# Performance work log

Measured on AMD Instinct MI355X. Metric: run time of the kernel, lower is better.

## Reference

```python
import jax, jax.numpy as jnp
import numpy as np

V, E, M, Q, K_ANS, L = 100000, 300, 256, 64, 1024, 64
T = K_ANS * L
WINDOW_SIZES = (1, 2, 3, 4, 5)


def setup_inputs() -> dict:
    key = jax.random.key(0)
    ks = jax.random.split(key, 16)
    s = 0.05
    inp = {
        "data_q": jax.random.randint(ks[0], (Q,), 0, V, dtype=jnp.int32),
        "data_as_word": jax.random.randint(ks[1], (T,), 0, V, dtype=jnp.int32),
        "sizes": jnp.full((K_ANS,), L, dtype=jnp.int32),
        "emb": jax.random.normal(ks[2], (V, E), jnp.float32) * s,
        "W1": jax.random.normal(ks[3], (E, M), jnp.float32) * s,
        "b1": jnp.zeros((M,), jnp.float32),
        "W2": jax.random.normal(ks[4], (E, M), jnp.float32) * s,
        "b2": jnp.zeros((M,), jnp.float32),
        "Wl": jax.random.normal(ks[5], (len(WINDOW_SIZES) * M, M), jnp.float32) * s,
        "bl": jnp.zeros((M,), jnp.float32),
        "Ws": jax.random.normal(ks[6], (M, 1), jnp.float32) * s,
        "bs": jnp.zeros((1,), jnp.float32),
    }
    for i, w in enumerate(WINDOW_SIZES):
        inp[f"Wc{i+1}"] = jax.random.normal(ks[7 + i], (M, M, w), jnp.float32) * s
        inp[f"bc{i+1}"] = jnp.zeros((M,), jnp.float32)
    return inp


def _dmax(c, sizes, w):
    # Dynamic max pool: c is [Lc, M] conv+relu over the concatenated answer axis;
    # each answer k owns conv positions [start_k, start_k + sizes_k - w + 1).
    starts = jnp.concatenate([jnp.zeros((1,), sizes.dtype), jnp.cumsum(sizes)[:-1]])
    pos = jnp.arange(c.shape[0])
    seg = jnp.searchsorted(starts, pos, side="right") - 1  # answer id per position
    valid = pos < starts[seg] + sizes[seg] - (w - 1)
    vals = jnp.where(valid[:, None], c, -jnp.inf)
    return jax.ops.segment_max(vals, seg, num_segments=sizes.shape[0])  # [K, M]


def reference(data_q, data_as_word, sizes, emb, W1, b1, W2, b2,
              Wc1, bc1, Wc2, bc2, Wc3, bc3, Wc4, bc4, Wc5, bc5, Wl, bl, Ws, bs):
    # Gated projection layer: sigmoid(Wx) * tanh(Wx)
    proj = lambda x: jax.nn.sigmoid(x @ W1 + b1) * jnp.tanh(x @ W2 + b2)
    q_p = proj(emb[data_q])        # [Q, M]
    a_p = proj(emb[data_as_word])  # [T, M]
    # Attention: mm -> softmax over dim 0 of attention.T -> mm (as in original)
    att = q_p @ a_p.T                       # [Q, T]
    w_att = jax.nn.softmax(att.T, axis=0)   # [T, Q]
    ctx = w_att @ q_p                       # [T, M]
    sim = a_p * ctx                         # compare step ('mul')  [T, M]
    # Conv + dynamic max pooling per window size
    x = sim.T[None]                         # [1, M, T]
    convs = ((Wc1, bc1), (Wc2, bc2), (Wc3, bc3), (Wc4, bc4), (Wc5, bc5))
    pools = []
    for wsz, (Wc, bc) in zip(WINDOW_SIZES, convs):
        c = jax.lax.conv_general_dilated(
            x, Wc, (1,), "VALID", dimension_numbers=("NCH", "OIH", "NCH"))[0].T  # [T-w+1, M]
        c = jax.nn.relu(c + bc)
        pools.append(_dmax(c, sizes, wsz))  # [K, M]
    h = jnp.tanh(jnp.concatenate(pools, axis=1) @ Wl + bl)  # [K, M]
    logits = (h @ Ws + bs).reshape(-1)                       # [K]
    return jax.nn.log_softmax(logits, axis=0)
```

## Files before the change

kernel.cpp:

```cpp
#include <hip/hip_runtime.h>

typedef unsigned short u16;
typedef unsigned int u32;
using s16x8 = __attribute__((ext_vector_type(8))) short;
using f32x4 = __attribute__((ext_vector_type(4))) float;
using u16x4 = __attribute__((ext_vector_type(4))) u16;

#define DEV __device__ __forceinline__

DEV u16 f2bf(float f) {
    u32 u = __builtin_bit_cast(u32, f);
    u32 r = (u + 0x7FFFu + ((u >> 16) & 1u)) >> 16;
    return (u16)r;
}
DEV float bf2f(u16 h) { return __builtin_bit_cast(float, ((u32)h) << 16); }

DEV f32x4 mfma16(s16x8 a, s16x8 b, f32x4 c) {
    return __builtin_amdgcn_mfma_f32_16x16x32_bf16(a, b, c, 0, 0, 0);
}

#define GLOAD(g, l) __builtin_amdgcn_global_load_lds( \
    (const __attribute__((address_space(1))) unsigned int*)(g), \
    (__attribute__((address_space(3))) unsigned int*)(l), 16, 0, 0)

__global__ void k_prep(const float* W1, const float* W2, const float* Wl,
                       const float* Wc1, const float* Wc2, const float* Wc3,
                       const float* Wc4, const float* Wc5,
                       u16* WpT, u16* WlT, u16* WcT) {
    int idx = blockIdx.x * 256 + threadIdx.x;
    if (idx < 512 * 320) {
        int n = idx / 320, k = idx - n * 320;
        float v = 0.f;
        if (k < 300) v = (n < 256) ? W1[k * 256 + n] : W2[k * 256 + (n - 256)];
        WpT[idx] = f2bf(v);
    } else if (idx < 512 * 320 + 256 * 1280) {
        int j2 = idx - 512 * 320;
        int m = j2 / 1280, j = j2 - m * 1280;
        WlT[j2] = f2bf(Wl[j * 256 + m]);
    } else {
        int j3 = idx - (512 * 320 + 256 * 1280);
        if (j3 < 983040) {
            int wsz; int off;
            if (j3 < 65536)       { wsz = 1; off = 0; }
            else if (j3 < 196608) { wsz = 2; off = 65536; }
            else if (j3 < 393216) { wsz = 3; off = 196608; }
            else if (j3 < 655360) { wsz = 4; off = 393216; }
            else                  { wsz = 5; off = 655360; }
            int loc = j3 - off;
            int o = loc / (256 * wsz);
            int kk = loc - o * (256 * wsz);
            int dw = kk >> 8, i = kk & 255;
            const float* W = (wsz == 1) ? Wc1 : (wsz == 2) ? Wc2 : (wsz == 3) ? Wc3
                             : (wsz == 4) ? Wc4 : Wc5;
            WcT[j3] = f2bf(W[(o * 256 + i) * wsz + dw]);
        }
    }
}

__global__ void k_starts(const int* sizes, int* starts) {
    __shared__ int s[1024];
    int t = threadIdx.x;
    int v = sizes[t];
    s[t] = v;
    __syncthreads();
    for (int off = 1; off < 1024; off <<= 1) {
        int add = (t >= off) ? s[t - off] : 0;
        __syncthreads();
        s[t] += add;
        __syncthreads();
    }
    starts[t] = s[t] - v;
}

__launch_bounds__(512)
__global__ void k_proj(const int* idx, const float* emb, const u16* WpT,
                       const float* b1, const float* b2, u16* out) {
    __shared__ u16 X[64 * 320];
    int tid = threadIdx.x;
    long row0 = (long)blockIdx.x * 64;
    {
        int r = tid >> 3, part = tid & 7;
        const float* src = emb + (long)idx[row0 + r] * 300;
        char* xrow = (char*)X + r * 640;
        u32 swz = (u32)((r & 7) << 4);
        for (int c0 = part * 40; c0 < part * 40 + 40; c0 += 4) {
            float4 f;
            if (c0 + 4 <= 300) f = *(const float4*)(src + c0);
            else {
                f.x = (c0 < 300) ? src[c0] : 0.f;
                f.y = (c0 + 1 < 300) ? src[c0 + 1] : 0.f;
                f.z = (c0 + 2 < 300) ? src[c0 + 2] : 0.f;
                f.w = (c0 + 3 < 300) ? src[c0 + 3] : 0.f;
            }
            u16x4 h = { f2bf(f.x), f2bf(f.y), f2bf(f.z), f2bf(f.w) };
            *(u16x4*)(xrow + ((u32)(c0 * 2) ^ swz)) = h;
        }
    }
    __syncthreads();
    int wv = tid >> 6, lane = tid & 63, l15 = lane & 15, lq = lane >> 4;
    f32x4 acc[4][4] = {};
    for (int s = 0; s < 10; ++s) {
        s16x8 a[4], b[4];
#pragma unroll
        for (int c = 0; c < 4; ++c) {
            int mt = 2 * wv + (c & 1) + (c >> 1) * 16;
            int o = mt * 16 + l15;
            a[c] = *(const s16x8*)(WpT + o * 320 + s * 32 + lq * 8);
        }
#pragma unroll
        for (int nt = 0; nt < 4; ++nt) {
            int r = nt * 16 + l15;
            b[nt] = *(const s16x8*)((const char*)X + r * 640 +
                                    ((u32)(s * 64 + lq * 16) ^ ((u32)(r & 7) << 4)));
        }
#pragma unroll
        for (int c = 0; c < 4; ++c)
#pragma unroll
            for (int nt = 0; nt < 4; ++nt)
                acc[c][nt] = mfma16(a[c], b[nt], acc[c][nt]);
    }
    __syncthreads();
    u16* Y = X;
#pragma unroll
    for (int c = 0; c < 2; ++c) {
        int o0 = (2 * wv + c) * 16 + lq * 4;
#pragma unroll
        for (int nt = 0; nt < 4; ++nt) {
            int t = nt * 16 + l15;
#pragma unroll
            for (int r = 0; r < 4; ++r) {
                float xs = acc[c][nt][r] + b1[o0 + r];
                float xt = acc[c + 2][nt][r] + b2[o0 + r];
                float v = (1.f / (1.f + __expf(-xs))) * tanhf(xt);
                Y[t * 256 + o0 + r] = f2bf(v);
            }
        }
    }
    __syncthreads();
    for (int j = tid; j < 2048; j += 512) {
        int t = j >> 5, c8 = (j & 31) * 8;
        *(s16x8*)(out + (row0 + t) * 256 + c8) = *(const s16x8*)(Y + t * 256 + c8);
    }
}

__launch_bounds__(256)
__global__ void k_att(const u16* qp, const u16* ap, float* att) {
    __shared__ u16 Q[64 * 256];
    __shared__ u16 A[64 * 256];
    int tid = threadIdx.x;
    long t0 = (long)blockIdx.x * 64;
    for (int j = tid; j < 2048; j += 256) {
        int r = j >> 5, c8 = (j & 31) * 8;
        u32 dst = (u32)(c8 * 2) ^ ((u32)(r & 7) << 4);
        *(s16x8*)((char*)Q + r * 512 + dst) = *(const s16x8*)(qp + r * 256 + c8);
        *(s16x8*)((char*)A + r * 512 + dst) = *(const s16x8*)(ap + (t0 + r) * 256 + c8);
    }
    __syncthreads();
    int wv = tid >> 6, lane = tid & 63, l15 = lane & 15, lq = lane >> 4;
    f32x4 acc[4] = {};
    for (int s = 0; s < 8; ++s) {
        int brow = wv * 16 + l15;
        s16x8 b = *(const s16x8*)((const char*)A + brow * 512 +
                                  ((u32)(s * 64 + lq * 16) ^ ((u32)(brow & 7) << 4)));
#pragma unroll
        for (int mt = 0; mt < 4; ++mt) {
            int arow = mt * 16 + l15;
            s16x8 a = *(const s16x8*)((const char*)Q + arow * 512 +
                                      ((u32)(s * 64 + lq * 16) ^ ((u32)(arow & 7) << 4)));
            acc[mt] = mfma16(a, b, acc[mt]);
        }
    }
#pragma unroll
    for (int mt = 0; mt < 4; ++mt) {
        long t = t0 + wv * 16 + l15;
        *(f32x4*)(att + t * 64 + mt * 16 + lq * 4) = acc[mt];
    }
}

__global__ void k_red1(const float* att, float* partm, float* parts) {
    int tid = threadIdx.x;
    int q = tid & 63, sub = tid >> 6;
    long t0 = (long)blockIdx.x * 512;
    float m = -3.0e38f, s = 0.f;
    for (int i = sub; i < 512; i += 4) {
        float v = att[(t0 + i) * 64 + q];
        if (v > m) { s = s * __expf(m - v) + 1.f; m = v; }
        else s += __expf(v - m);
    }
    __shared__ float Lm[4][64], Ls[4][64];
    Lm[sub][q] = m; Ls[sub][q] = s;
    __syncthreads();
    if (sub == 0) {
        for (int i = 1; i < 4; ++i) {
            float m2 = Lm[i][q], s2 = Ls[i][q];
            float mn = fmaxf(m, m2);
            s = s * __expf(m - mn) + s2 * __expf(m2 - mn);
            m = mn;
        }
        partm[blockIdx.x * 64 + q] = m;
        parts[blockIdx.x * 64 + q] = s;
    }
}

__global__ void k_red2(const float* partm, const float* parts, float* mx, float* rden) {
    int q = threadIdx.x;
    float m = -3.0e38f, s = 0.f;
    for (int b = 0; b < 128; ++b) {
        float m2 = partm[b * 64 + q], s2 = parts[b * 64 + q];
        float mn = fmaxf(m, m2);
        s = s * __expf(m - mn) + s2 * __expf(m2 - mn);
        m = mn;
    }
    mx[q] = m;
    rden[q] = 1.f / s;
}

__launch_bounds__(256)
__global__ void k_ctx(const float* att, const float* mx, const float* rden,
                      const u16* qp, const u16* ap, u16* sim) {
    __shared__ u16 P[64 * 64];
    __shared__ u16 QT[256 * 64];
    __shared__ u16 Y[64 * 264];
    __shared__ float MX[64], RD[64];
    int tid = threadIdx.x;
    long t0 = (long)blockIdx.x * 64;
    if (tid < 64) { MX[tid] = mx[tid]; RD[tid] = rden[tid]; }
    {
        int m = tid;
        char* row = (char*)QT + m * 128;
        u32 swz = (u32)((m & 7) << 4);
        for (int q = 0; q < 64; ++q)
            *(u16*)(row + ((u32)(q * 2) ^ swz)) = qp[q * 256 + m];
    }
    __syncthreads();
    {
        int t = tid >> 2, qq = tid & 3;
        const float* arow = att + (t0 + t) * 64 + qq * 16;
        char* prow = (char*)P + t * 128;
        u32 swz = (u32)((t & 7) << 4);
#pragma unroll
        for (int i4 = 0; i4 < 4; ++i4) {
            float4 fv = *(const float4*)(arow + i4 * 4);
            int q0 = qq * 16 + i4 * 4;
            float p0 = __expf(fv.x - MX[q0 + 0]) * RD[q0 + 0];
            float p1 = __expf(fv.y - MX[q0 + 1]) * RD[q0 + 1];
            float p2 = __expf(fv.z - MX[q0 + 2]) * RD[q0 + 2];
            float p3 = __expf(fv.w - MX[q0 + 3]) * RD[q0 + 3];
            *(u16*)(prow + ((u32)((q0 + 0) * 2) ^ swz)) = f2bf(p0);
            *(u16*)(prow + ((u32)((q0 + 1) * 2) ^ swz)) = f2bf(p1);
            *(u16*)(prow + ((u32)((q0 + 2) * 2) ^ swz)) = f2bf(p2);
            *(u16*)(prow + ((u32)((q0 + 3) * 2) ^ swz)) = f2bf(p3);
        }
    }
    __syncthreads();
    int wv = tid >> 6, lane = tid & 63, l15 = lane & 15, lq = lane >> 4;
    f32x4 acc[16] = {};
#pragma unroll
    for (int s = 0; s < 2; ++s) {
        int arow = wv * 16 + l15;
        s16x8 a = *(const s16x8*)((const char*)P + arow * 128 +
                                  ((u32)(s * 64 + lq * 16) ^ ((u32)(arow & 7) << 4)));
#pragma unroll
        for (int nt = 0; nt < 16; ++nt) {
            int br = nt * 16 + l15;
            s16x8 b = *(const s16x8*)((const char*)QT + br * 128 +
                                      ((u32)(s * 64 + lq * 16) ^ ((u32)(br & 7) << 4)));
            acc[nt] = mfma16(a, b, acc[nt]);
        }
    }
#pragma unroll
    for (int nt = 0; nt < 16; ++nt) {
        int m = nt * 16 + l15;
        int t = wv * 16 + lq * 4;
#pragma unroll
        for (int r = 0; r < 4; ++r) Y[(t + r) * 264 + m] = f2bf(acc[nt][r]);
    }
    __syncthreads();
    for (int j = tid; j < 2048; j += 256) {
        int t = j >> 5, c8 = (j & 31) * 8;
        s16x8 y = *(const s16x8*)(Y + t * 264 + c8);
        s16x8 a8 = *(const s16x8*)(ap + (t0 + t) * 256 + c8);
        s16x8 o;
#pragma unroll
        for (int e = 0; e < 8; ++e)
            o[e] = (short)f2bf(bf2f((u16)a8[e]) * bf2f((u16)y[e]));
        *(s16x8*)(sim + (t0 + t) * 256 + c8) = o;
    }
}

__launch_bounds__(512)
__global__ void k_conv(const u16* sim, const u16* WcT,
                       const int* starts, const int* sizes,
                       const float* bc1, const float* bc2, const float* bc3,
                       const float* bc4, const float* bc5,
                       u16* pools, int Ttot) {
    __shared__ u16 LB[2][32768];
    int tid = threadIdx.x;
    int wv = tid >> 6, lane = tid & 63, l15 = lane & 15, lq = lane >> 4;
    int wm = wv >> 2, wn = wv & 3;
    int b = blockIdx.x;
    long s0 = starts[4 * b];
    int row8 = lane >> 3, seg = lane & 7;
    u32 sA = ((u32)(seg * 16)) ^ (((u32)(row8 & 7)) << 4);

    auto STAGE = [&](int nb, int w_, int dw_, int ic_) {
        int Krow = 256 * w_;
        long wbase = 65536L * ((w_ * (w_ - 1)) / 2);
#pragma unroll
        for (int it = 0; it < 4; ++it) {
            int c = wv * 4 + it;
            long g = s0 + dw_ + c * 8 + row8;
            if (g >= Ttot) g = Ttot - 1;
            const char* srcA = (const char*)sim + g * 512 + ic_ * 128 + sA;
            GLOAD(srcA, (char*)LB[nb] + c * 1024);
        }
#pragma unroll
        for (int it = 0; it < 4; ++it) {
            int c = wv * 4 + it;
            int o = c * 8 + row8;
            const char* srcB = (const char*)WcT +
                2L * (wbase + (long)o * Krow + dw_ * 256 + ic_ * 64) + sA;
            GLOAD(srcB, (char*)LB[nb] + 32768 + c * 1024);
        }
    };
    auto ADV = [](int& w_, int& dw_, int& ic_) {
        if (++ic_ == 4) { ic_ = 0; if (++dw_ == w_) { dw_ = 0; ++w_; } }
    };

    int wS = 1, dwS = 0, icS = 0;
    STAGE(0, wS, dwS, icS);
    ADV(wS, dwS, icS);
    __syncthreads();

    int buf = 0;
    f32x4 acc[8][4] = {};
    int wC = 1, dwC = 0, icC = 0;
    for (int t = 0; t < 60; ++t) {
        if (t < 59) { STAGE(buf ^ 1, wS, dwS, icS); ADV(wS, dwS, icS); }
        const char* Ab = (const char*)LB[buf];
        const char* Bb = (const char*)LB[buf] + 32768;
#pragma unroll
        for (int ks = 0; ks < 2; ++ks) {
            s16x8 A8[8], B4[4];
#pragma unroll
            for (int mt = 0; mt < 8; ++mt) {
                int row = wm * 128 + mt * 16 + l15;
                A8[mt] = *(const s16x8*)(Ab + row * 128 +
                          (((u32)(ks * 64 + lq * 16)) ^ (((u32)(row & 7)) << 4)));
            }
#pragma unroll
            for (int nt = 0; nt < 4; ++nt) {
                int o = wn * 64 + nt * 16 + l15;
                B4[nt] = *(const s16x8*)(Bb + o * 128 +
                          (((u32)(ks * 64 + lq * 16)) ^ (((u32)(o & 7)) << 4)));
            }
            __builtin_amdgcn_s_setprio(1);
#pragma unroll
            for (int mt = 0; mt < 8; ++mt)
#pragma unroll
                for (int nt = 0; nt < 4; ++nt)
                    acc[mt][nt] = mfma16(A8[mt], B4[nt], acc[mt][nt]);
            __builtin_amdgcn_s_setprio(0);
        }
        if (++icC == 4) {
            icC = 0;
            if (++dwC == wC) {
                dwC = 0;
                const float* bc = (wC == 1) ? bc1 : (wC == 2) ? bc2 : (wC == 3) ? bc3
                                  : (wC == 4) ? bc4 : bc5;
#pragma unroll
                for (int a2 = 0; a2 < 2; ++a2) {
                    int kans = b * 4 + wm * 2 + a2;
                    int valid = sizes[kans] - wC + 1;
#pragma unroll
                    for (int nt = 0; nt < 4; ++nt) {
                        float m = -3.0e38f;
#pragma unroll
                        for (int mth = 0; mth < 4; ++mth) {
                            int mt = a2 * 4 + mth;
#pragma unroll
                            for (int r = 0; r < 4; ++r) {
                                int pp = mth * 16 + lq * 4 + r;
                                float v = (pp < valid) ? acc[mt][nt][r] : -3.0e38f;
                                m = fmaxf(m, v);
                            }
                        }
                        m = fmaxf(m, __shfl_xor(m, 16, 64));
                        m = fmaxf(m, __shfl_xor(m, 32, 64));
                        if (lq == 0) {
                            int o = wn * 64 + nt * 16 + l15;
                            float pool = fmaxf(m + bc[o], 0.f);
                            pools[(long)kans * 1280 + (wC - 1) * 256 + o] = f2bf(pool);
                        }
                    }
                }
#pragma unroll
                for (int mt = 0; mt < 8; ++mt)
#pragma unroll
                    for (int nt = 0; nt < 4; ++nt)
                        acc[mt][nt] = f32x4{0.f, 0.f, 0.f, 0.f};
                ++wC;
            }
        }
        __syncthreads();
        buf ^= 1;
    }
}

__launch_bounds__(256)
__global__ void k_head(const u16* pools, const u16* WlT,
                       const float* bl, const float* Ws, const float* bs,
                       float* logits) {
    int tid = threadIdx.x;
    int k0 = blockIdx.x * 64;
    int wv = tid >> 6, lane = tid & 63, l15 = lane & 15, lq = lane >> 4;
    f32x4 acc[4][4] = {};
    for (int s = 0; s < 40; ++s) {
        s16x8 a[4], b[4];
#pragma unroll
        for (int mt = 0; mt < 4; ++mt) {
            int m = (wv * 4 + mt) * 16 + l15;
            a[mt] = *(const s16x8*)(WlT + (long)m * 1280 + s * 32 + lq * 8);
        }
#pragma unroll
        for (int nt = 0; nt < 4; ++nt) {
            int kk = k0 + nt * 16 + l15;
            b[nt] = *(const s16x8*)(pools + (long)kk * 1280 + s * 32 + lq * 8);
        }
#pragma unroll
        for (int mt = 0; mt < 4; ++mt)
#pragma unroll
            for (int nt = 0; nt < 4; ++nt)
                acc[mt][nt] = mfma16(a[mt], b[nt], acc[mt][nt]);
    }
    __shared__ float PS[4][4][16];
#pragma unroll
    for (int nt = 0; nt < 4; ++nt) {
        float p = 0.f;
#pragma unroll
        for (int mt = 0; mt < 4; ++mt) {
            int m0 = (wv * 4 + mt) * 16 + lq * 4;
#pragma unroll
            for (int r = 0; r < 4; ++r) {
                float h = tanhf(acc[mt][nt][r] + bl[m0 + r]);
                p += h * Ws[m0 + r];
            }
        }
        p += __shfl_xor(p, 16, 64);
        p += __shfl_xor(p, 32, 64);
        if (lq == 0) PS[wv][nt][l15] = p;
    }
    __syncthreads();
    if (tid < 64) {
        int nt = tid >> 4, i = tid & 15;
        float v = PS[0][nt][i] + PS[1][nt][i] + PS[2][nt][i] + PS[3][nt][i] + bs[0];
        logits[k0 + nt * 16 + i] = v;
    }
}

__global__ void k_lsm(const float* logits, float* out) {
    __shared__ float r1[16], r2[16];
    int tid = threadIdx.x;
    float v = logits[tid];
    float m = v;
#pragma unroll
    for (int off = 32; off >= 1; off >>= 1) m = fmaxf(m, __shfl_xor(m, off, 64));
    if ((tid & 63) == 0) r1[tid >> 6] = m;
    __syncthreads();
    if (tid < 16) {
        float t = r1[tid];
#pragma unroll
        for (int off = 8; off >= 1; off >>= 1) t = fmaxf(t, __shfl_xor(t, off, 64));
        r1[tid] = t;
    }
    __syncthreads();
    m = r1[0];
    float e = __expf(v - m);
    float s = e;
#pragma unroll
    for (int off = 32; off >= 1; off >>= 1) s += __shfl_xor(s, off, 64);
    if ((tid & 63) == 0) r2[tid >> 6] = s;
    __syncthreads();
    if (tid < 16) {
        float t = r2[tid];
#pragma unroll
        for (int off = 8; off >= 1; off >>= 1) t += __shfl_xor(t, off, 64);
        r2[tid] = t;
    }
    __syncthreads();
    out[tid] = v - m - logf(r2[0]);
}

extern "C" void kernel_launch(void* const* d_in, const int* in_sizes, int n_in,
                              void* d_out, int out_size, void* d_ws, size_t ws_size,
                              hipStream_t stream) {
    const int*   data_q  = (const int*)d_in[0];
    const int*   data_as = (const int*)d_in[1];
    const int*   sizes   = (const int*)d_in[2];
    const float* emb = (const float*)d_in[3];
    const float* W1  = (const float*)d_in[4];
    const float* b1  = (const float*)d_in[5];
    const float* W2  = (const float*)d_in[6];
    const float* b2  = (const float*)d_in[7];
    const float* Wl  = (const float*)d_in[8];
    const float* bl  = (const float*)d_in[9];
    const float* Ws  = (const float*)d_in[10];
    const float* bs  = (const float*)d_in[11];
    const float* Wc1 = (const float*)d_in[12]; const float* bc1 = (const float*)d_in[13];
    const float* Wc2 = (const float*)d_in[14]; const float* bc2 = (const float*)d_in[15];
    const float* Wc3 = (const float*)d_in[16]; const float* bc3 = (const float*)d_in[17];
    const float* Wc4 = (const float*)d_in[18]; const float* bc4 = (const float*)d_in[19];
    const float* Wc5 = (const float*)d_in[20]; const float* bc5 = (const float*)d_in[21];
    int Ttot = in_sizes[1];

    char* ws = (char*)d_ws;
    u16*   WpT    = (u16*)  (ws + 0);
    u16*   WlT    = (u16*)  (ws + 327680);
    u16*   WcT    = (u16*)  (ws + 983040);
    u16*   qp     = (u16*)  (ws + 2949120);
    u16*   ap     = (u16*)  (ws + 2981888);
    float* att    = (float*)(ws + 36536320);
    float* partm  = (float*)(ws + 53313536);
    float* parts  = (float*)(ws + 53346304);
    float* mx     = (float*)(ws + 53379072);
    float* rden   = (float*)(ws + 53379328);
    u16*   sim    = (u16*)  (ws + 53379584);
    u16*   pools  = (u16*)  (ws + 86934016);
    float* logits = (float*)(ws + 89555456);
    int*   starts = (int*)  (ws + 89559552);

    k_prep<<<5760, 256, 0, stream>>>(W1, W2, Wl, Wc1, Wc2, Wc3, Wc4, Wc5, WpT, WlT, WcT);
    k_starts<<<1, 1024, 0, stream>>>(sizes, starts);
    k_proj<<<1024, 512, 0, stream>>>(data_as, emb, WpT, b1, b2, ap);
    k_proj<<<1, 512, 0, stream>>>(data_q, emb, WpT, b1, b2, qp);
    k_att<<<1024, 256, 0, stream>>>(qp, ap, att);
    k_red1<<<128, 256, 0, stream>>>(att, partm, parts);
    k_red2<<<1, 64, 0, stream>>>(partm, parts, mx, rden);
    k_ctx<<<1024, 256, 0, stream>>>(att, mx, rden, qp, ap, sim);
    k_conv<<<256, 512, 0, stream>>>(sim, WcT, starts, sizes, bc1, bc2, bc3, bc4, bc5,
                                    pools, Ttot);
    k_head<<<16, 256, 0, stream>>>(pools, WlT, bl, Ws, bs, logits);
    k_lsm<<<1, 1024, 0, stream>>>(logits, (float*)d_out);
}
```

Baseline: 349.4 us.

## Fuse softmax partial reduction into attention kernel and retile conv for more blocks

The column-wise online softmax partial max/sum is now computed inside k_att from a shared-memory copy of each 64-row tile, which removes the k_red1 launch and its re-read of the attention matrix. k_red2 is widened to 512 threads to merge the 1024 partials. The conv kernel is retiled from 4 answers per 512-thread block to 2 answers per block, doubling the grid to 512 blocks. It uses a smaller K-step of 32 with a new LDS swizzle, cutting shared memory per block and allowing more resident blocks, at the cost of twice as many pipeline iterations and barriers. The partial buffers reuse the pools region, which is safe only because pools is written after k_red2 has finished.

```diff
diff --git a/kernel.cpp b/kernel.cpp
--- a/kernel.cpp
+++ b/kernel.cpp
@@ -144,9 +144,12 @@
 }
 
 __launch_bounds__(256)
-__global__ void k_att(const u16* qp, const u16* ap, float* att) {
+__global__ void k_att(const u16* qp, const u16* ap, float* att,
+                      float* partm, float* parts) {
     __shared__ u16 Q[64 * 256];
     __shared__ u16 A[64 * 256];
+    __shared__ float AT[64][68];
+    __shared__ float Lm[4][64], Ls[4][64];
     int tid = threadIdx.x;
     long t0 = (long)blockIdx.x * 64;
     for (int j = tid; j < 2048; j += 256) {
@@ -170,27 +173,29 @@
             acc[mt] = mfma16(a, b, acc[mt]);
         }
     }
+    int t = wv * 16 + l15;
 #pragma unroll
     for (int mt = 0; mt < 4; ++mt) {
-        long t = t0 + wv * 16 + l15;
-        *(f32x4*)(att + t * 64 + mt * 16 + lq * 4) = acc[mt];
-    }
-}
-
-__global__ void k_red1(const float* att, float* partm, float* parts) {
-    int tid = threadIdx.x;
-    int q = tid & 63, sub = tid >> 6;
-    long t0 = (long)blockIdx.x * 512;
-    float m = -3.0e38f, s = 0.f;
-    for (int i = sub; i < 512; i += 4) {
-        float v = att[(t0 + i) * 64 + q];
-        if (v > m) { s = s * __expf(m - v) + 1.f; m = v; }
-        else s += __expf(v - m);
-    }
-    __shared__ float Lm[4][64], Ls[4][64];
-    Lm[sub][q] = m; Ls[sub][q] = s;
-    __syncthreads();
-    if (sub == 0) {
+        *(f32x4*)(att + (t0 + t) * 64 + mt * 16 + lq * 4) = acc[mt];
+        *(f32x4*)&AT[t][mt * 16 + lq * 4] = acc[mt];
+    }
+    __syncthreads();
+    {
+        int q = tid & 63, sub = tid >> 6;
+        float m = -3.0e38f, s = 0.f;
+#pragma unroll
+        for (int i = 0; i < 16; ++i) {
+            float v = AT[sub * 16 + i][q];
+            if (v > m) { s = s * __expf(m - v) + 1.f; m = v; }
+            else s += __expf(v - m);
+        }
+        Lm[sub][q] = m; Ls[sub][q] = s;
+    }
+    __syncthreads();
+    if (tid < 64) {
+        int q = tid;
+        float m = Lm[0][q], s = Ls[0][q];
+#pragma unroll
         for (int i = 1; i < 4; ++i) {
             float m2 = Lm[i][q], s2 = Ls[i][q];
             float mn = fmaxf(m, m2);
@@ -202,17 +207,30 @@
     }
 }
 
+__launch_bounds__(512)
 __global__ void k_red2(const float* partm, const float* parts, float* mx, float* rden) {
-    int q = threadIdx.x;
+    __shared__ float Lm[8][64], Ls[8][64];
+    int q = threadIdx.x & 63, sub = threadIdx.x >> 6;
     float m = -3.0e38f, s = 0.f;
-    for (int b = 0; b < 128; ++b) {
+    for (int b = sub; b < 1024; b += 8) {
         float m2 = partm[b * 64 + q], s2 = parts[b * 64 + q];
         float mn = fmaxf(m, m2);
         s = s * __expf(m - mn) + s2 * __expf(m2 - mn);
         m = mn;
     }
-    mx[q] = m;
-    rden[q] = 1.f / s;
+    Lm[sub][q] = m; Ls[sub][q] = s;
+    __syncthreads();
+    if (sub == 0) {
+#pragma unroll
+        for (int i = 1; i < 8; ++i) {
+            float m2 = Lm[i][q], s2 = Ls[i][q];
+            float mn = fmaxf(m, m2);
+            s = s * __expf(m - mn) + s2 * __expf(m2 - mn);
+            m = mn;
+        }
+        mx[q] = m;
+        rden[q] = 1.f / s;
+    }
 }
 
 __launch_bounds__(256)
@@ -288,43 +306,41 @@
     }
 }
 
-__launch_bounds__(512)
+__launch_bounds__(512, 4)
 __global__ void k_conv(const u16* sim, const u16* WcT,
                        const int* starts, const int* sizes,
                        const float* bc1, const float* bc2, const float* bc3,
                        const float* bc4, const float* bc5,
                        u16* pools, int Ttot) {
-    __shared__ u16 LB[2][32768];
+    __shared__ u16 AB[2][12288];
     int tid = threadIdx.x;
     int wv = tid >> 6, lane = tid & 63, l15 = lane & 15, lq = lane >> 4;
     int wm = wv >> 2, wn = wv & 3;
     int b = blockIdx.x;
-    long s0 = starts[4 * b];
-    int row8 = lane >> 3, seg = lane & 7;
-    u32 sA = ((u32)(seg * 16)) ^ (((u32)(row8 & 7)) << 4);
+    long s0 = starts[2 * b];
+    int rc = lane >> 2;
+    int p4 = lane & 3;
+    int ksg = (p4 - (rc >> 1)) & 3;
 
     auto STAGE = [&](int nb, int w_, int dw_, int ic_) {
         int Krow = 256 * w_;
         long wbase = 65536L * ((w_ * (w_ - 1)) / 2);
-#pragma unroll
-        for (int it = 0; it < 4; ++it) {
-            int c = wv * 4 + it;
-            long g = s0 + dw_ + c * 8 + row8;
+        {
+            long g = s0 + dw_ + wv * 16 + rc;
             if (g >= Ttot) g = Ttot - 1;
-            const char* srcA = (const char*)sim + g * 512 + ic_ * 128 + sA;
-            GLOAD(srcA, (char*)LB[nb] + c * 1024);
-        }
-#pragma unroll
-        for (int it = 0; it < 4; ++it) {
-            int c = wv * 4 + it;
-            int o = c * 8 + row8;
+            const char* srcA = (const char*)sim + g * 512 + ic_ * 64 + ksg * 16;
+            GLOAD(srcA, (char*)AB[nb] + wv * 1024);
+        }
+#pragma unroll
+        for (int h = 0; h < 2; ++h) {
+            int o = wv * 32 + h * 16 + rc;
             const char* srcB = (const char*)WcT +
-                2L * (wbase + (long)o * Krow + dw_ * 256 + ic_ * 64) + sA;
-            GLOAD(srcB, (char*)LB[nb] + 32768 + c * 1024);
+                2L * (wbase + (long)o * Krow + dw_ * 256 + ic_ * 32) + ksg * 16;
+            GLOAD(srcB, (char*)AB[nb] + 8192 + (wv * 2 + h) * 1024);
         }
     };
     auto ADV = [](int& w_, int& dw_, int& ic_) {
-        if (++ic_ == 4) { ic_ = 0; if (++dw_ == w_) { dw_ = 0; ++w_; } }
+        if (++ic_ == 8) { ic_ = 0; if (++dw_ == w_) { dw_ = 0; ++w_; } }
     };
 
     int wS = 1, dwS = 0, icS = 0;
@@ -333,69 +349,57 @@
     __syncthreads();
 
     int buf = 0;
-    f32x4 acc[8][4] = {};
+    f32x4 acc[4][4] = {};
     int wC = 1, dwC = 0, icC = 0;
-    for (int t = 0; t < 60; ++t) {
-        if (t < 59) { STAGE(buf ^ 1, wS, dwS, icS); ADV(wS, dwS, icS); }
-        const char* Ab = (const char*)LB[buf];
-        const char* Bb = (const char*)LB[buf] + 32768;
-#pragma unroll
-        for (int ks = 0; ks < 2; ++ks) {
-            s16x8 A8[8], B4[4];
-#pragma unroll
-            for (int mt = 0; mt < 8; ++mt) {
-                int row = wm * 128 + mt * 16 + l15;
-                A8[mt] = *(const s16x8*)(Ab + row * 128 +
-                          (((u32)(ks * 64 + lq * 16)) ^ (((u32)(row & 7)) << 4)));
-            }
-#pragma unroll
-            for (int nt = 0; nt < 4; ++nt) {
-                int o = wn * 64 + nt * 16 + l15;
-                B4[nt] = *(const s16x8*)(Bb + o * 128 +
-                          (((u32)(ks * 64 + lq * 16)) ^ (((u32)(o & 7)) << 4)));
-            }
-            __builtin_amdgcn_s_setprio(1);
-#pragma unroll
-            for (int mt = 0; mt < 8; ++mt)
-#pragma unroll
-                for (int nt = 0; nt < 4; ++nt)
-                    acc[mt][nt] = mfma16(A8[mt], B4[nt], acc[mt][nt]);
-            __builtin_amdgcn_s_setprio(0);
-        }
-        if (++icC == 4) {
+    u32 gsl = (u32)(((lq + (l15 >> 1)) & 3) * 16);
+    for (int t = 0; t < 120; ++t) {
+        if (t < 119) { STAGE(buf ^ 1, wS, dwS, icS); ADV(wS, dwS, icS); }
+        const char* Ab = (const char*)AB[buf];
+        const char* Bb = (const char*)AB[buf] + 8192;
+        s16x8 A4[4], B4[4];
+#pragma unroll
+        for (int mt = 0; mt < 4; ++mt)
+            A4[mt] = *(const s16x8*)(Ab + (wm * 4 + mt) * 1024 + l15 * 64 + gsl);
+#pragma unroll
+        for (int nt = 0; nt < 4; ++nt)
+            B4[nt] = *(const s16x8*)(Bb + (wn * 4 + nt) * 1024 + l15 * 64 + gsl);
+        __builtin_amdgcn_s_setprio(1);
+#pragma unroll
+        for (int mt = 0; mt < 4; ++mt)
+#pragma unroll
+            for (int nt = 0; nt < 4; ++nt)
+                acc[mt][nt] = mfma16(A4[mt], B4[nt], acc[mt][nt]);
+        __builtin_amdgcn_s_setprio(0);
+        if (++icC == 8) {
             icC = 0;
             if (++dwC == wC) {
                 dwC = 0;
                 const float* bc = (wC == 1) ? bc1 : (wC == 2) ? bc2 : (wC == 3) ? bc3
                                   : (wC == 4) ? bc4 : bc5;
-#pragma unroll
-                for (int a2 = 0; a2 < 2; ++a2) {
-                    int kans = b * 4 + wm * 2 + a2;
-                    int valid = sizes[kans] - wC + 1;
-#pragma unroll
-                    for (int nt = 0; nt < 4; ++nt) {
-                        float m = -3.0e38f;
-#pragma unroll
-                        for (int mth = 0; mth < 4; ++mth) {
-                            int mt = a2 * 4 + mth;
-#pragma unroll
-                            for (int r = 0; r < 4; ++r) {
-                                int pp = mth * 16 + lq * 4 + r;
-                                float v = (pp < valid) ? acc[mt][nt][r] : -3.0e38f;
-                                m = fmaxf(m, v);
-                            }
-                        }
-                        m = fmaxf(m, __shfl_xor(m, 16, 64));
-                        m = fmaxf(m, __shfl_xor(m, 32, 64));
-                        if (lq == 0) {
-                            int o = wn * 64 + nt * 16 + l15;
-                            float pool = fmaxf(m + bc[o], 0.f);
-                            pools[(long)kans * 1280 + (wC - 1) * 256 + o] = f2bf(pool);
+                int kans = 2 * b + wm;
+                int valid = sizes[kans] - wC + 1;
+#pragma unroll
+                for (int nt = 0; nt < 4; ++nt) {
+                    float m = -3.0e38f;
+#pragma unroll
+                    for (int mt = 0; mt < 4; ++mt) {
+#pragma unroll
+                        for (int r = 0; r < 4; ++r) {
+                            int pp = mt * 16 + lq * 4 + r;
+                            float v = (pp < valid) ? acc[mt][nt][r] : -3.0e38f;
+                            m = fmaxf(m, v);
                         }
                     }
+                    m = fmaxf(m, __shfl_xor(m, 16, 64));
+                    m = fmaxf(m, __shfl_xor(m, 32, 64));
+                    if (lq == 0) {
+                        int o = wn * 64 + nt * 16 + l15;
+                        float pool = fmaxf(m + bc[o], 0.f);
+                        pools[(long)kans * 1280 + (wC - 1) * 256 + o] = f2bf(pool);
+                    }
                 }
 #pragma unroll
-                for (int mt = 0; mt < 8; ++mt)
+                for (int mt = 0; mt < 4; ++mt)
 #pragma unroll
                     for (int nt = 0; nt < 4; ++nt)
                         acc[mt][nt] = f32x4{0.f, 0.f, 0.f, 0.f};
@@ -520,24 +524,23 @@
     u16*   qp     = (u16*)  (ws + 2949120);
     u16*   ap     = (u16*)  (ws + 2981888);
     float* att    = (float*)(ws + 36536320);
-    float* partm  = (float*)(ws + 53313536);
-    float* parts  = (float*)(ws + 53346304);
     float* mx     = (float*)(ws + 53379072);
     float* rden   = (float*)(ws + 53379328);
     u16*   sim    = (u16*)  (ws + 53379584);
     u16*   pools  = (u16*)  (ws + 86934016);
     float* logits = (float*)(ws + 89555456);
     int*   starts = (int*)  (ws + 89559552);
+    float* partm  = (float*)pools;
+    float* parts  = (float*)((char*)pools + 262144);
 
     k_prep<<<5760, 256, 0, stream>>>(W1, W2, Wl, Wc1, Wc2, Wc3, Wc4, Wc5, WpT, WlT, WcT);
     k_starts<<<1, 1024, 0, stream>>>(sizes, starts);
     k_proj<<<1024, 512, 0, stream>>>(data_as, emb, WpT, b1, b2, ap);
     k_proj<<<1, 512, 0, stream>>>(data_q, emb, WpT, b1, b2, qp);
-    k_att<<<1024, 256, 0, stream>>>(qp, ap, att);
-    k_red1<<<128, 256, 0, stream>>>(att, partm, parts);
-    k_red2<<<1, 64, 0, stream>>>(partm, parts, mx, rden);
+    k_att<<<1024, 256, 0, stream>>>(qp, ap, att, partm, parts);
+    k_red2<<<1, 512, 0, stream>>>(partm, parts, mx, rden);
     k_ctx<<<1024, 256, 0, stream>>>(att, mx, rden, qp, ap, sim);
-    k_conv<<<256, 512, 0, stream>>>(sim, WcT, starts, sizes, bc1, bc2, bc3, bc4, bc5,
+    k_conv<<<512, 512, 0, stream>>>(sim, WcT, starts, sizes, bc1, bc2, bc3, bc4, bc5,
                                     pools, Ttot);
     k_head<<<16, 256, 0, stream>>>(pools, WlT, bl, Ws, bs, logits);
     k_lsm<<<1, 1024, 0, stream>>>(logits, (float*)d_out);
```

Result: slower. 373.2 us (+6.8%).

## Fuse softmax partial reduction into attention kernel and pre-transpose query projection

Applied to the files above, without the earlier changes.

Computes per-block softmax partial max/sum inside k_att from an LDS copy of the scores, which removes the separate k_red1 pass that re-read the whole att matrix. k_red2 is widened to reduce 1024 partials with 512 threads. A small k_qpt kernel transposes qp once, so k_ctx no longer rebuilds a transposed Q in LDS in every block, and k_att/k_ctx read operands straight from global memory instead of staging them in LDS. The costs are uncoalesced direct global loads for the MFMA operands and reuse of the pools buffer as scratch for the partials.

```diff
diff --git a/kernel.cpp b/kernel.cpp
--- a/kernel.cpp
+++ b/kernel.cpp
@@ -72,6 +72,23 @@
     starts[t] = s[t] - v;
 }
 
+__global__ void k_qpt(const u16* qp, u16* qpT) {
+    __shared__ u16 L[64 * 260];
+    int tid = threadIdx.x;
+    for (int j = tid; j < 2048; j += 256) {
+        int q = j >> 5, c8 = (j & 31) * 8;
+        *(s16x8*)(L + q * 260 + c8) = *(const s16x8*)(qp + q * 256 + c8);
+    }
+    __syncthreads();
+    int m = tid;
+    u16 buf[64];
+#pragma unroll
+    for (int q = 0; q < 64; ++q) buf[q] = L[q * 260 + m];
+#pragma unroll
+    for (int h = 0; h < 8; ++h)
+        *(s16x8*)(qpT + m * 64 + h * 8) = *(const s16x8*)(buf + h * 8);
+}
+
 __launch_bounds__(512)
 __global__ void k_proj(const int* idx, const float* emb, const u16* WpT,
                        const float* b1, const float* b2, u16* out) {
@@ -144,53 +161,47 @@
 }
 
 __launch_bounds__(256)
-__global__ void k_att(const u16* qp, const u16* ap, float* att) {
-    __shared__ u16 Q[64 * 256];
-    __shared__ u16 A[64 * 256];
+__global__ void k_att(const u16* qp, const u16* ap, float* att,
+                      float* partm, float* parts) {
+    __shared__ float AT[64][68];
+    __shared__ float Lm[4][64], Ls[4][64];
     int tid = threadIdx.x;
     long t0 = (long)blockIdx.x * 64;
-    for (int j = tid; j < 2048; j += 256) {
-        int r = j >> 5, c8 = (j & 31) * 8;
-        u32 dst = (u32)(c8 * 2) ^ ((u32)(r & 7) << 4);
-        *(s16x8*)((char*)Q + r * 512 + dst) = *(const s16x8*)(qp + r * 256 + c8);
-        *(s16x8*)((char*)A + r * 512 + dst) = *(const s16x8*)(ap + (t0 + r) * 256 + c8);
-    }
-    __syncthreads();
     int wv = tid >> 6, lane = tid & 63, l15 = lane & 15, lq = lane >> 4;
     f32x4 acc[4] = {};
+    const u16* brow = ap + (t0 + wv * 16 + l15) * 256 + lq * 8;
+    const u16* arow = qp + l15 * 256 + lq * 8;
     for (int s = 0; s < 8; ++s) {
-        int brow = wv * 16 + l15;
-        s16x8 b = *(const s16x8*)((const char*)A + brow * 512 +
-                                  ((u32)(s * 64 + lq * 16) ^ ((u32)(brow & 7) << 4)));
+        s16x8 b = *(const s16x8*)(brow + s * 32);
 #pragma unroll
         for (int mt = 0; mt < 4; ++mt) {
-            int arow = mt * 16 + l15;
-            s16x8 a = *(const s16x8*)((const char*)Q + arow * 512 +
-                                      ((u32)(s * 64 + lq * 16) ^ ((u32)(arow & 7) << 4)));
+            s16x8 a = *(const s16x8*)(arow + mt * 16 * 256 + s * 32);
             acc[mt] = mfma16(a, b, acc[mt]);
         }
     }
+    int t = wv * 16 + l15;
 #pragma unroll
     for (int mt = 0; mt < 4; ++mt) {
-        long t = t0 + wv * 16 + l15;
-        *(f32x4*)(att + t * 64 + mt * 16 + lq * 4) = acc[mt];
-    }
-}
-
-__global__ void k_red1(const float* att, float* partm, float* parts) {
-    int tid = threadIdx.x;
-    int q = tid & 63, sub = tid >> 6;
-    long t0 = (long)blockIdx.x * 512;
-    float m = -3.0e38f, s = 0.f;
-    for (int i = sub; i < 512; i += 4) {
-        float v = att[(t0 + i) * 64 + q];
-        if (v > m) { s = s * __expf(m - v) + 1.f; m = v; }
-        else s += __expf(v - m);
-    }
-    __shared__ float Lm[4][64], Ls[4][64];
-    Lm[sub][q] = m; Ls[sub][q] = s;
-    __syncthreads();
-    if (sub == 0) {
+        *(f32x4*)(att + (t0 + t) * 64 + mt * 16 + lq * 4) = acc[mt];
+        *(f32x4*)&AT[t][mt * 16 + lq * 4] = acc[mt];
+    }
+    __syncthreads();
+    {
+        int q = tid & 63, sub = tid >> 6;
+        float m = -3.0e38f, s = 0.f;
+#pragma unroll
+        for (int i = 0; i < 16; ++i) {
+            float v = AT[sub * 16 + i][q];
+            if (v > m) { s = s * __expf(m - v) + 1.f; m = v; }
+            else s += __expf(v - m);
+        }
+        Lm[sub][q] = m; Ls[sub][q] = s;
+    }
+    __syncthreads();
+    if (tid < 64) {
+        int q = tid;
+        float m = Lm[0][q], s = Ls[0][q];
+#pragma unroll
         for (int i = 1; i < 4; ++i) {
             float m2 = Lm[i][q], s2 = Ls[i][q];
             float mn = fmaxf(m, m2);
@@ -202,69 +213,59 @@
     }
 }
 
+__launch_bounds__(512)
 __global__ void k_red2(const float* partm, const float* parts, float* mx, float* rden) {
-    int q = threadIdx.x;
+    __shared__ float Lm[8][64], Ls[8][64];
+    int q = threadIdx.x & 63, sub = threadIdx.x >> 6;
     float m = -3.0e38f, s = 0.f;
-    for (int b = 0; b < 128; ++b) {
+    for (int b = sub; b < 1024; b += 8) {
         float m2 = partm[b * 64 + q], s2 = parts[b * 64 + q];
         float mn = fmaxf(m, m2);
         s = s * __expf(m - mn) + s2 * __expf(m2 - mn);
         m = mn;
     }
-    mx[q] = m;
-    rden[q] = 1.f / s;
+    Lm[sub][q] = m; Ls[sub][q] = s;
+    __syncthreads();
+    if (sub == 0) {
+#pragma unroll
+        for (int i = 1; i < 8; ++i) {
+            float m2 = Lm[i][q], s2 = Ls[i][q];
+            float mn = fmaxf(m, m2);
+            s = s * __expf(m - mn) + s2 * __expf(m2 - mn);
+            m = mn;
+        }
+        mx[q] = m;
+        rden[q] = 1.f / s;
+    }
 }
 
 __launch_bounds__(256)
 __global__ void k_ctx(const float* att, const float* mx, const float* rden,
-                      const u16* qp, const u16* ap, u16* sim) {
-    __shared__ u16 P[64 * 64];
-    __shared__ u16 QT[256 * 64];
+                      const u16* qpT, const u16* ap, u16* sim) {
     __shared__ u16 Y[64 * 264];
-    __shared__ float MX[64], RD[64];
     int tid = threadIdx.x;
     long t0 = (long)blockIdx.x * 64;
-    if (tid < 64) { MX[tid] = mx[tid]; RD[tid] = rden[tid]; }
-    {
-        int m = tid;
-        char* row = (char*)QT + m * 128;
-        u32 swz = (u32)((m & 7) << 4);
-        for (int q = 0; q < 64; ++q)
-            *(u16*)(row + ((u32)(q * 2) ^ swz)) = qp[q * 256 + m];
-    }
-    __syncthreads();
-    {
-        int t = tid >> 2, qq = tid & 3;
-        const float* arow = att + (t0 + t) * 64 + qq * 16;
-        char* prow = (char*)P + t * 128;
-        u32 swz = (u32)((t & 7) << 4);
-#pragma unroll
-        for (int i4 = 0; i4 < 4; ++i4) {
-            float4 fv = *(const float4*)(arow + i4 * 4);
-            int q0 = qq * 16 + i4 * 4;
-            float p0 = __expf(fv.x - MX[q0 + 0]) * RD[q0 + 0];
-            float p1 = __expf(fv.y - MX[q0 + 1]) * RD[q0 + 1];
-            float p2 = __expf(fv.z - MX[q0 + 2]) * RD[q0 + 2];
-            float p3 = __expf(fv.w - MX[q0 + 3]) * RD[q0 + 3];
-            *(u16*)(prow + ((u32)((q0 + 0) * 2) ^ swz)) = f2bf(p0);
-            *(u16*)(prow + ((u32)((q0 + 1) * 2) ^ swz)) = f2bf(p1);
-            *(u16*)(prow + ((u32)((q0 + 2) * 2) ^ swz)) = f2bf(p2);
-            *(u16*)(prow + ((u32)((q0 + 3) * 2) ^ swz)) = f2bf(p3);
-        }
-    }
-    __syncthreads();
     int wv = tid >> 6, lane = tid & 63, l15 = lane & 15, lq = lane >> 4;
     f32x4 acc[16] = {};
 #pragma unroll
     for (int s = 0; s < 2; ++s) {
-        int arow = wv * 16 + l15;
-        s16x8 a = *(const s16x8*)((const char*)P + arow * 128 +
-                                  ((u32)(s * 64 + lq * 16) ^ ((u32)(arow & 7) << 4)));
+        int q0 = s * 32 + lq * 8;
+        const float* arow = att + (t0 + wv * 16 + l15) * 64 + q0;
+        f32x4 v0 = *(const f32x4*)(arow);
+        f32x4 v1 = *(const f32x4*)(arow + 4);
+        f32x4 m0 = *(const f32x4*)(mx + q0);
+        f32x4 m1 = *(const f32x4*)(mx + q0 + 4);
+        f32x4 r0 = *(const f32x4*)(rden + q0);
+        f32x4 r1 = *(const f32x4*)(rden + q0 + 4);
+        s16x8 a;
+#pragma unroll
+        for (int e = 0; e < 4; ++e) {
+            a[e]     = (short)f2bf(__expf(v0[e] - m0[e]) * r0[e]);
+            a[e + 4] = (short)f2bf(__expf(v1[e] - m1[e]) * r1[e]);
+        }
 #pragma unroll
         for (int nt = 0; nt < 16; ++nt) {
-            int br = nt * 16 + l15;
-            s16x8 b = *(const s16x8*)((const char*)QT + br * 128 +
-                                      ((u32)(s * 64 + lq * 16) ^ ((u32)(br & 7) << 4)));
+            s16x8 b = *(const s16x8*)(qpT + (nt * 16 + l15) * 64 + q0);
             acc[nt] = mfma16(a, b, acc[nt]);
         }
     }
@@ -520,23 +521,24 @@
     u16*   qp     = (u16*)  (ws + 2949120);
     u16*   ap     = (u16*)  (ws + 2981888);
     float* att    = (float*)(ws + 36536320);
-    float* partm  = (float*)(ws + 53313536);
-    float* parts  = (float*)(ws + 53346304);
     float* mx     = (float*)(ws + 53379072);
     float* rden   = (float*)(ws + 53379328);
     u16*   sim    = (u16*)  (ws + 53379584);
     u16*   pools  = (u16*)  (ws + 86934016);
     float* logits = (float*)(ws + 89555456);
     int*   starts = (int*)  (ws + 89559552);
+    u16*   qpT    = (u16*)  (ws + 89563648);
+    float* partm  = (float*)pools;
+    float* parts  = (float*)((char*)pools + 262144);
 
     k_prep<<<5760, 256, 0, stream>>>(W1, W2, Wl, Wc1, Wc2, Wc3, Wc4, Wc5, WpT, WlT, WcT);
     k_starts<<<1, 1024, 0, stream>>>(sizes, starts);
     k_proj<<<1024, 512, 0, stream>>>(data_as, emb, WpT, b1, b2, ap);
     k_proj<<<1, 512, 0, stream>>>(data_q, emb, WpT, b1, b2, qp);
-    k_att<<<1024, 256, 0, stream>>>(qp, ap, att);
-    k_red1<<<128, 256, 0, stream>>>(att, partm, parts);
-    k_red2<<<1, 64, 0, stream>>>(partm, parts, mx, rden);
-    k_ctx<<<1024, 256, 0, stream>>>(att, mx, rden, qp, ap, sim);
+    k_qpt<<<1, 256, 0, stream>>>(qp, qpT);
+    k_att<<<1024, 256, 0, stream>>>(qp, ap, att, partm, parts);
+    k_red2<<<1, 512, 0, stream>>>(partm, parts, mx, rden);
+    k_ctx<<<1024, 256, 0, stream>>>(att, mx, rden, qpT, ap, sim);
     k_conv<<<256, 512, 0, stream>>>(sim, WcT, starts, sizes, bc1, bc2, bc3, bc4, bc5,
                                     pools, Ttot);
     k_head<<<16, 256, 0, stream>>>(pools, WlT, bl, Ws, bs, logits);
```

New measurement: 369.0 us. +5.6%, slower.

## Fuse softmax partial reductions into attention kernel and merge small launches

Applied to the files above, without the earlier changes.

Folds the per-block softmax max/sum partials into the attention matmul kernel, computed from registers with wave shuffles and shared memory, so the separate pass that re-read the full attention matrix is removed. The prefix-sum of sizes moves into an extra block of the weight-prep kernel, and the query projection becomes one extra block of the answer projection launch, cutting three kernel launches. The final reduction now combines 1024 partials with 512 threads, and the partial buffers reuse the pools workspace, which relies on pools being written only after those partials are consumed.

```diff
diff --git a/kernel.cpp b/kernel.cpp
--- a/kernel.cpp
+++ b/kernel.cpp
@@ -26,8 +26,30 @@
 __global__ void k_prep(const float* W1, const float* W2, const float* Wl,
                        const float* Wc1, const float* Wc2, const float* Wc3,
                        const float* Wc4, const float* Wc5,
-                       u16* WpT, u16* WlT, u16* WcT) {
-    int idx = blockIdx.x * 256 + threadIdx.x;
+                       u16* WpT, u16* WlT, u16* WcT,
+                       const int* sizes, int* starts) {
+    int tid = threadIdx.x;
+    if (blockIdx.x == 5760) {
+        __shared__ int ps[256];
+        int t4 = tid * 4;
+        int v0 = sizes[t4], v1 = sizes[t4 + 1], v2 = sizes[t4 + 2], v3 = sizes[t4 + 3];
+        int sum = v0 + v1 + v2 + v3;
+        ps[tid] = sum;
+        __syncthreads();
+        for (int off = 1; off < 256; off <<= 1) {
+            int add = (tid >= off) ? ps[tid - off] : 0;
+            __syncthreads();
+            ps[tid] += add;
+            __syncthreads();
+        }
+        int base = tid ? ps[tid - 1] : 0;
+        starts[t4] = base;
+        starts[t4 + 1] = base + v0;
+        starts[t4 + 2] = base + v0 + v1;
+        starts[t4 + 3] = base + v0 + v1 + v2;
+        return;
+    }
+    int idx = blockIdx.x * 256 + tid;
     if (idx < 512 * 320) {
         int n = idx / 320, k = idx - n * 320;
         float v = 0.f;
@@ -57,27 +79,16 @@
     }
 }
 
-__global__ void k_starts(const int* sizes, int* starts) {
-    __shared__ int s[1024];
-    int t = threadIdx.x;
-    int v = sizes[t];
-    s[t] = v;
-    __syncthreads();
-    for (int off = 1; off < 1024; off <<= 1) {
-        int add = (t >= off) ? s[t - off] : 0;
-        __syncthreads();
-        s[t] += add;
-        __syncthreads();
-    }
-    starts[t] = s[t] - v;
-}
-
 __launch_bounds__(512)
-__global__ void k_proj(const int* idx, const float* emb, const u16* WpT,
-                       const float* b1, const float* b2, u16* out) {
+__global__ void k_proj(const int* data_as, const int* data_q, const float* emb,
+                       const u16* WpT, const float* b1, const float* b2,
+                       u16* ap, u16* qp) {
     __shared__ u16 X[64 * 320];
     int tid = threadIdx.x;
-    long row0 = (long)blockIdx.x * 64;
+    bool isq = (blockIdx.x == 1024);
+    const int* idx = isq ? data_q : data_as;
+    u16* out = isq ? qp : ap;
+    long row0 = isq ? 0 : (long)blockIdx.x * 64;
     {
         int r = tid >> 3, part = tid & 7;
         const float* src = emb + (long)idx[row0 + r] * 300;
@@ -144,9 +155,11 @@
 }
 
 __launch_bounds__(256)
-__global__ void k_att(const u16* qp, const u16* ap, float* att) {
+__global__ void k_att(const u16* qp, const u16* ap, float* att,
+                      float* partm, float* parts) {
     __shared__ u16 Q[64 * 256];
     __shared__ u16 A[64 * 256];
+    __shared__ float Pm[8][64], Ps[8][64], Qm[64];
     int tid = threadIdx.x;
     long t0 = (long)blockIdx.x * 64;
     for (int j = tid; j < 2048; j += 256) {
@@ -175,44 +188,85 @@
         long t = t0 + wv * 16 + l15;
         *(f32x4*)(att + t * 64 + mt * 16 + lq * 4) = acc[mt];
     }
-}
-
-__global__ void k_red1(const float* att, float* partm, float* parts) {
-    int tid = threadIdx.x;
-    int q = tid & 63, sub = tid >> 6;
-    long t0 = (long)blockIdx.x * 512;
+    float mxv[16];
+#pragma unroll
+    for (int mt = 0; mt < 4; ++mt)
+#pragma unroll
+        for (int r = 0; r < 4; ++r) mxv[mt * 4 + r] = acc[mt][r];
+#pragma unroll
+    for (int off = 1; off <= 8; off <<= 1)
+#pragma unroll
+        for (int i = 0; i < 16; ++i)
+            mxv[i] = fmaxf(mxv[i], __shfl_xor(mxv[i], off, 64));
+    if (l15 == 0) {
+#pragma unroll
+        for (int mt = 0; mt < 4; ++mt)
+#pragma unroll
+            for (int r = 0; r < 4; ++r)
+                Pm[wv][mt * 16 + lq * 4 + r] = mxv[mt * 4 + r];
+    }
+    __syncthreads();
+    if (tid < 64) {
+        float g = Pm[0][tid];
+#pragma unroll
+        for (int i = 1; i < 8; ++i) g = fmaxf(g, Pm[i][tid]);
+        Qm[tid] = g;
+    }
+    __syncthreads();
+    float sv[16];
+#pragma unroll
+    for (int mt = 0; mt < 4; ++mt)
+#pragma unroll
+        for (int r = 0; r < 4; ++r) {
+            int q = mt * 16 + lq * 4 + r;
+            sv[mt * 4 + r] = __expf(acc[mt][r] - Qm[q]);
+        }
+#pragma unroll
+    for (int off = 1; off <= 8; off <<= 1)
+#pragma unroll
+        for (int i = 0; i < 16; ++i)
+            sv[i] += __shfl_xor(sv[i], off, 64);
+    if (l15 == 0) {
+#pragma unroll
+        for (int mt = 0; mt < 4; ++mt)
+#pragma unroll
+            for (int r = 0; r < 4; ++r)
+                Ps[wv][mt * 16 + lq * 4 + r] = sv[mt * 4 + r];
+    }
+    __syncthreads();
+    if (tid < 64) {
+        float s = Ps[0][tid];
+#pragma unroll
+        for (int i = 1; i < 8; ++i) s += Ps[i][tid];
+        partm[blockIdx.x * 64 + tid] = Qm[tid];
+        parts[blockIdx.x * 64 + tid] = s;
+    }
+}
+
+__launch_bounds__(512)
+__global__ void k_red2(const float* partm, const float* parts, float* mx, float* rden) {
+    __shared__ float Lm[8][64], Ls[8][64];
+    int q = threadIdx.x & 63, sub = threadIdx.x >> 6;
     float m = -3.0e38f, s = 0.f;
-    for (int i = sub; i < 512; i += 4) {
-        float v = att[(t0 + i) * 64 + q];
-        if (v > m) { s = s * __expf(m - v) + 1.f; m = v; }
-        else s += __expf(v - m);
-    }
-    __shared__ float Lm[4][64], Ls[4][64];
+    for (int b = sub; b < 1024; b += 8) {
+        float m2 = partm[b * 64 + q], s2 = parts[b * 64 + q];
+        float mn = fmaxf(m, m2);
+        s = s * __expf(m - mn) + s2 * __expf(m2 - mn);
+        m = mn;
+    }
     Lm[sub][q] = m; Ls[sub][q] = s;
     __syncthreads();
     if (sub == 0) {
-        for (int i = 1; i < 4; ++i) {
+#pragma unroll
+        for (int i = 1; i < 8; ++i) {
             float m2 = Lm[i][q], s2 = Ls[i][q];
             float mn = fmaxf(m, m2);
             s = s * __expf(m - mn) + s2 * __expf(m2 - mn);
             m = mn;
         }
-        partm[blockIdx.x * 64 + q] = m;
-        parts[blockIdx.x * 64 + q] = s;
-    }
-}
-
-__global__ void k_red2(const float* partm, const float* parts, float* mx, float* rden) {
-    int q = threadIdx.x;
-    float m = -3.0e38f, s = 0.f;
-    for (int b = 0; b < 128; ++b) {
-        float m2 = partm[b * 64 + q], s2 = parts[b * 64 + q];
-        float mn = fmaxf(m, m2);
-        s = s * __expf(m - mn) + s2 * __expf(m2 - mn);
-        m = mn;
-    }
-    mx[q] = m;
-    rden[q] = 1.f / s;
+        mx[q] = m;
+        rden[q] = 1.f / s;
+    }
 }
 
 __launch_bounds__(256)
@@ -520,22 +574,20 @@
     u16*   qp     = (u16*)  (ws + 2949120);
     u16*   ap     = (u16*)  (ws + 2981888);
     float* att    = (float*)(ws + 36536320);
-    float* partm  = (float*)(ws + 53313536);
-    float* parts  = (float*)(ws + 53346304);
     float* mx     = (float*)(ws + 53379072);
     float* rden   = (float*)(ws + 53379328);
     u16*   sim    = (u16*)  (ws + 53379584);
     u16*   pools  = (u16*)  (ws + 86934016);
     float* logits = (float*)(ws + 89555456);
     int*   starts = (int*)  (ws + 89559552);
-
-    k_prep<<<5760, 256, 0, stream>>>(W1, W2, Wl, Wc1, Wc2, Wc3, Wc4, Wc5, WpT, WlT, WcT);
-    k_starts<<<1, 1024, 0, stream>>>(sizes, starts);
-    k_proj<<<1024, 512, 0, stream>>>(data_as, emb, WpT, b1, b2, ap);
-    k_proj<<<1, 512, 0, stream>>>(data_q, emb, WpT, b1, b2, qp);
-    k_att<<<1024, 256, 0, stream>>>(qp, ap, att);
-    k_red1<<<128, 256, 0, stream>>>(att, partm, parts);
-    k_red2<<<1, 64, 0, stream>>>(partm, parts, mx, rden);
+    float* partm  = (float*)pools;
+    float* parts  = (float*)((char*)pools + 262144);
+
+    k_prep<<<5761, 256, 0, stream>>>(W1, W2, Wl, Wc1, Wc2, Wc3, Wc4, Wc5,
+                                     WpT, WlT, WcT, sizes, starts);
+    k_proj<<<1025, 512, 0, stream>>>(data_as, data_q, emb, WpT, b1, b2, ap, qp);
+    k_att<<<1024, 256, 0, stream>>>(qp, ap, att, partm, parts);
+    k_red2<<<1, 512, 0, stream>>>(partm, parts, mx, rden);
     k_ctx<<<1024, 256, 0, stream>>>(att, mx, rden, qp, ap, sim);
     k_conv<<<256, 512, 0, stream>>>(sim, WcT, starts, sizes, bc1, bc2, bc3, bc4, bc5,
                                     pools, Ttot);
```

After: 340.4 us. 1.03x faster.
